# Performance work log

Measured on AMD Instinct MI355X. Metric: run time of the kernel, lower is better.

Reference implementation:

```python
import jax, jax.numpy as jnp
import numpy as np

N_NODES = 40000
N_EDGES = 640000
C = 64
NUM_GAUSS = 50
RBF_STOP = 5.0


def silu(x):
    return x * jax.nn.sigmoid(x)


def setup_inputs() -> dict:
    key = jax.random.key(0)
    ks = jax.random.split(key, 16)
    scalar = jax.random.normal(ks[0], (N_NODES, C), dtype=jnp.float32)
    vector = jax.random.normal(ks[1], (N_NODES, 3, C), dtype=jnp.float32)
    position = jax.random.normal(ks[2], (N_NODES, 3), dtype=jnp.float32)
    # avoid self-edges so dist > 0 (sqrt grad finite in bwd variant)
    row = jax.random.randint(ks[3], (N_EDGES,), 0, N_NODES, dtype=jnp.int32)
    off = jax.random.randint(ks[4], (N_EDGES,), 1, N_NODES, dtype=jnp.int32)
    col = (row + off) % N_NODES
    edge_index = jnp.stack([row, col], axis=0)
    edge_attr = jax.random.uniform(ks[5], (N_EDGES,), dtype=jnp.float32) + 0.1
    s = 1.0 / np.sqrt(2 * C)
    Ws2s = jax.random.normal(ks[6], (2 * C, C), dtype=jnp.float32) * s
    bs2s = jnp.zeros((C,), dtype=jnp.float32)
    Wv2s = jax.random.normal(ks[7], (2 * C + NUM_GAUSS, C), dtype=jnp.float32) * s
    bv2s = jnp.zeros((C,), dtype=jnp.float32)
    Wsl = jax.random.normal(ks[8], (2 * C, C), dtype=jnp.float32) * s
    bsl = jnp.zeros((C,), dtype=jnp.float32)
    Ws2v = jax.random.normal(ks[9], (2 * C, C), dtype=jnp.float32) * s
    bs2v = jnp.zeros((C,), dtype=jnp.float32)
    Wv2v = jax.random.normal(ks[10], (2 * C, C), dtype=jnp.float32) * s
    Wvl = jax.random.normal(ks[11], (2 * C, C), dtype=jnp.float32) * s
    return dict(scalar=scalar, vector=vector, position=position,
                edge_index=edge_index, edge_attr=edge_attr,
                Ws2s=Ws2s, bs2s=bs2s, Wv2s=Wv2s, bv2s=bv2s,
                Wsl=Wsl, bsl=bsl, Ws2v=Ws2v, bs2v=bs2v, Wv2v=Wv2v, Wvl=Wvl)


def _molnet_layer(scalar, vector, position, edge_index, edge_attr,
                  Ws2s, bs2s, Wv2s, bv2s, Wsl, bsl, Ws2v, bs2v, Wv2v, Wvl):
    N = scalar.shape[0]
    row, col = edge_index[0], edge_index[1]
    # B=True degree normalization: deg[c] = sum of edge_attr into c
    deg = jax.ops.segment_sum(edge_attr, col, num_segments=N)
    dis = jnp.where(deg > 0, deg ** -0.5, 0.0)
    norm = dis[row] * dis[col] * edge_attr  # [E]

    # PyG convention: _i = target (col), _j = source (row)
    si, sj = scalar[col], scalar[row]          # [E, C]
    vi, vj = vector[col], vector[row]          # [E, 3, C]
    pi, pj = position[col], position[row]      # [E, 3]

    rel = pi - pj                              # [E, 3]
    dist = jnp.sqrt(jnp.sum(rel * rel, axis=-1))  # [E]

    # GaussianSmearing(0, 5, 50)
    offset = jnp.linspace(0.0, RBF_STOP, NUM_GAUSS, dtype=scalar.dtype)
    coeff = -0.5 / (RBF_STOP / (NUM_GAUSS - 1)) ** 2
    rbf = jnp.exp(coeff * (dist[:, None] - offset[None, :]) ** 2)  # [E, 50]

    # ---- Scalar_Conv message ----
    ss = silu(jnp.concatenate([si, sj], axis=1) @ Ws2s + bs2s)  # [E, C]
    vn_i = jnp.linalg.norm(vi, axis=1)  # [E, C], norm over 3-axis
    vn_j = jnp.linalg.norm(vj, axis=1)
    vs = silu(jnp.concatenate([vn_i, vn_j, rbf], axis=-1) @ Wv2s + bv2s)  # [E, C]
    msg_s = norm[:, None] * (jnp.concatenate([ss, vs], axis=1) @ Wsl + bsl)
    agg_s = jax.ops.segment_sum(msg_s, col, num_segments=N)  # [N, C]

    # ---- Vector_Conv message ----
    vv = jnp.concatenate([vi, vj], axis=-1) @ Wv2v  # [E, 3, C], no bias
    sv = jnp.tanh(jnp.concatenate([si, sj], axis=1) @ Ws2v + bs2v)  # [E, C]
    sv = sv[:, None, :] * rel[:, :, None]  # [E, 3, C]
    msg_v = norm[:, None, None] * (jnp.concatenate([vv, sv], axis=-1) @ Wvl)
    agg_v = jax.ops.segment_sum(msg_v, col, num_segments=N)  # [N, 3, C]

    scalar_out = silu(agg_s) + scalar
    vector_out = agg_v + vector
    return scalar_out, vector_out


def reference(scalar, vector, position, edge_index, edge_attr,
              Ws2s, bs2s, Wv2s, bv2s, Wsl, bsl, Ws2v, bs2v, Wv2v, Wvl):
    return _molnet_layer(scalar, vector, position, edge_index, edge_attr,
                         Ws2s, bs2s, Wv2s, bv2s, Wsl, bsl, Ws2v, bs2v, Wv2v, Wvl)
```

## Files before the change

### kernel.cpp

```cpp
#include <hip/hip_runtime.h>


typedef __attribute__((ext_vector_type(8))) short bf16x8;
typedef __attribute__((ext_vector_type(4))) float f32x4;
#define MFMA16(a, b, c) __builtin_amdgcn_mfma_f32_16x16x32_bf16(a, b, c, 0, 0, 0)

__device__ __forceinline__ unsigned short f2bf(float x) {
    union { float f; unsigned u; } v; v.f = x;
    unsigned r = v.u + 0x7FFF + ((v.u >> 16) & 1);
    return (unsigned short)(r >> 16);
}
__device__ __forceinline__ float bf2f(unsigned short h) {
    union { unsigned u; float f; } v; v.u = ((unsigned)h) << 16; return v.f;
}
__device__ __forceinline__ float ulo(unsigned u) {
    union { unsigned u; float f; } v; v.u = u << 16; return v.f;
}
__device__ __forceinline__ float uhi(unsigned u) {
    union { unsigned u; float f; } v; v.u = u & 0xffff0000u; return v.f;
}
__device__ __forceinline__ float silu_f(float x) {
    return x * __builtin_amdgcn_rcpf(1.0f + __expf(-x));
}
__device__ __forceinline__ float tanh_f(float x) {
    return 1.0f - 2.0f * __builtin_amdgcn_rcpf(1.0f + __expf(2.0f * x));
}
__device__ __forceinline__ int rfl(int x) { return __builtin_amdgcn_readfirstlane(x); }

__global__ __launch_bounds__(256) void deg_cnt_k(const int* __restrict__ ei,
                                                 const float* __restrict__ attr,
                                                 float* __restrict__ dc, int E) {
    int e = blockIdx.x * 256 + threadIdx.x;
    if (e < E) {
        int col = ei[E + e];
        atomicAdd(&dc[2 * col], attr[e]);
        atomicAdd((int*)dc + 2 * col + 1, 1);
    }
}

__global__ __launch_bounds__(1024) void scan1_k(const float* __restrict__ dc,
                                                int* __restrict__ blockSums, int N) {
    __shared__ int tmp[1024];
    int i = blockIdx.x * 1024 + threadIdx.x;
    tmp[threadIdx.x] = (i < N) ? ((const int*)dc)[2 * i + 1] : 0;
    __syncthreads();
    for (int s = 512; s > 0; s >>= 1) {
        if (threadIdx.x < s) tmp[threadIdx.x] += tmp[threadIdx.x + s];
        __syncthreads();
    }
    if (threadIdx.x == 0) blockSums[blockIdx.x] = tmp[0];
}

__global__ __launch_bounds__(1024) void scan3_k(const float* __restrict__ dc,
                                                const int* __restrict__ blockSums,
                                                int* __restrict__ offA,
                                                int* __restrict__ offB,
                                                float* __restrict__ dis, int N) {
    __shared__ int tmp[1024];
    __shared__ int base_s;
    if (threadIdx.x == 0) {
        int b = 0;
        for (int j = 0; j < (int)blockIdx.x; ++j) b += blockSums[j];
        base_s = b;
    }
    int i = blockIdx.x * 1024 + threadIdx.x;
    tmp[threadIdx.x] = (i < N) ? ((const int*)dc)[2 * i + 1] : 0;
    __syncthreads();
    for (int s = 1; s < 1024; s <<= 1) {
        int t = (threadIdx.x >= s) ? tmp[threadIdx.x - s] : 0;
        __syncthreads();
        tmp[threadIdx.x] += t;
        __syncthreads();
    }
    if (i < N) {
        int off = base_s + tmp[threadIdx.x];
        offA[i + 1] = off;
        offB[i + 1] = off;
        float d = dc[2 * i];
        dis[i] = (d > 0.0f) ? rsqrtf(d) : 0.0f;
    }
    if (blockIdx.x == 0 && threadIdx.x == 0) { offA[0] = 0; offB[0] = 0; }
}

__global__ __launch_bounds__(256) void mid_k(
    const int* __restrict__ ei, const float* __restrict__ attr,
    const float* __restrict__ pos,
    const float* __restrict__ dis, int* __restrict__ offA,
    int2* __restrict__ PLa, float4* __restrict__ PLb, int E,
    const float* __restrict__ scalar, const float* __restrict__ vec,
    unsigned short* __restrict__ X, unsigned short* __restrict__ R2, int N,
    const float* __restrict__ Ws2s, const float* __restrict__ Ws2v,
    const float* __restrict__ Wv2s, const float* __restrict__ Wsl,
    const float* __restrict__ Wvl, const float* __restrict__ Wv2v,
    unsigned short* __restrict__ BT6, unsigned short* __restrict__ BTs,
    unsigned short* __restrict__ BTv, float* __restrict__ T2) {
    int idx = blockIdx.x * 256 + threadIdx.x;
    if (idx < E) {
        int row = ei[idx];
        int col = ei[E + idx];
        int p = atomicAdd(&offA[col], 1);
        float nrm = dis[col] * (dis[row] * attr[idx]);
        float r0 = pos[col * 3 + 0] - pos[row * 3 + 0];
        float r1 = pos[col * 3 + 1] - pos[row * 3 + 1];
        float r2 = pos[col * 3 + 2] - pos[row * 3 + 2];
        float d2 = r0 * r0 + r1 * r1 + r2 * r2;
        float t = fminf(sqrtf(d2) * (512.0f / 6.0f), 511.0f);
        PLa[p] = make_int2(row * 192, __float_as_int(nrm));
        PLb[p] = make_float4(r0, r1, r2, t);
        return;
    }
    idx -= E;
    if (idx < N * 64) {
        int n = idx >> 6, c = idx & 63;
        float v0 = vec[(size_t)n * 192 + c];
        float v1 = vec[(size_t)n * 192 + 64 + c];
        float v2 = vec[(size_t)n * 192 + 128 + c];
        X[(size_t)n * 128 + c] = f2bf(scalar[(size_t)n * 64 + c]);
        X[(size_t)n * 128 + 64 + c] = f2bf(sqrtf(v0 * v0 + v1 * v1 + v2 * v2));
        unsigned short* rw = R2 + (size_t)n * 384 + c * 6;
        rw[3] = f2bf(v0);
        *(unsigned*)(rw + 4) = (unsigned)f2bf(v1) | ((unsigned)f2bf(v2) << 16);
        return;
    }
    idx -= N * 64;
    if (idx < 24576) {
        int y = idx >> 12, n = (idx >> 6) & 63, k = idx & 63;
        const float* W = (y < 2) ? Ws2s : (y < 4) ? Ws2v : Wv2s;
        int kk = (y & 1) ? (64 + k) : k;
        BT6[idx] = f2bf(W[kk * 64 + n]);
    } else if (idx < 32768) {
        int j = idx - 24576;
        int n = j >> 7, k = j & 127;
        BTs[(size_t)n * 128 + k] = f2bf(Wsl[k * 64 + n]);
    } else if (idx < 36864) {
        int j = idx - 32768;
        int n = j >> 6, k = j & 63;
        BTv[(size_t)n * 192 + k] = f2bf(Wvl[(64 + k) * 64 + n]);
    } else if (idx < 45056) {
        int j = idx - 36864;
        int half = j >> 12;
        int k = (j >> 6) & 63, c = j & 63;
        const float* Wr = Wv2v + (half ? 0 : 64 * 64) + k * 64;
        float acc = 0.0f;
        for (int m = 0; m < 64; ++m) acc += Wr[m] * Wvl[m * 64 + c];
        BTv[(size_t)c * 192 + (half ? 128 : 64) + k] = f2bf(acc);
    } else {
        int j = idx - 45056;
        if (j >= 513 * 64) return;
        int s = j >> 6, c = j & 63;
        float d = (float)s * (6.0f / 512.0f);
        float acc = 0.0f;
        for (int l = 0; l < 50; ++l) {
            float dl = d - 0.10204081632653061f * (float)l;
            acc += __expf(-48.02f * dl * dl) * Wv2s[(128 + l) * 64 + c];
        }
        T2[(s * 64 + c) * 2] = acc;
        if (s > 0) T2[((s - 1) * 64 + c) * 2 + 1] = acc;
    }
}

__global__ __launch_bounds__(256) void node_gemm_k(
    const unsigned short* __restrict__ X, const unsigned short* __restrict__ BT6,
    const float* __restrict__ bs2s, const float* __restrict__ bs2v,
    const float* __restrict__ bv2s,
    unsigned short* __restrict__ PC3, unsigned short* __restrict__ R2, int N) {
    const int lane = threadIdx.x & 63;
    const int mtile = blockIdx.x * 4 + (threadIdx.x >> 6);
    const int r0 = mtile * 16;
    if (r0 >= N) return;
    const int quad = lane >> 4, l = lane & 15;
    const int arow = min(r0 + l, N - 1);
    const unsigned short* ap = X + (size_t)arow * 128 + quad * 8;
    bf16x8 as0 = *(const bf16x8*)ap;
    bf16x8 as1 = *(const bf16x8*)(ap + 32);
    bf16x8 av0 = *(const bf16x8*)(ap + 64);
    bf16x8 av1 = *(const bf16x8*)(ap + 96);
    f32x4 acc[6][4];
#pragma unroll
    for (int y = 0; y < 6; ++y) {
        bf16x8 a0 = (y < 4) ? as0 : av0;
        bf16x8 a1 = (y < 4) ? as1 : av1;
        const unsigned short* bp = BT6 + (size_t)y * 4096 + (size_t)l * 64 + quad * 8;
#pragma unroll
        for (int nt = 0; nt < 4; ++nt) {
            acc[y][nt] = (f32x4){0.f, 0.f, 0.f, 0.f};
            bf16x8 b0 = *(const bf16x8*)(bp + nt * 1024);
            bf16x8 b1 = *(const bf16x8*)(bp + nt * 1024 + 32);
            acc[y][nt] = MFMA16(a0, b0, acc[y][nt]);
            acc[y][nt] = MFMA16(a1, b1, acc[y][nt]);
        }
    }
#pragma unroll
    for (int nt = 0; nt < 4; ++nt) {
        int col = nt * 16 + l;
        float b0 = bs2s[col], b1 = bs2v[col], b2 = bv2s[col];
#pragma unroll
        for (int i = 0; i < 4; ++i) {
            int row = r0 + quad * 4 + i;
            if (row < N) {
                unsigned short* pd = PC3 + (size_t)row * 192 + col * 3;
                pd[0] = f2bf(acc[0][nt][i] + b0);
                pd[1] = f2bf(acc[2][nt][i] + b1);
                pd[2] = f2bf(acc[4][nt][i] + b2);
                unsigned short* rd = R2 + (size_t)row * 384 + col * 6;
                *(unsigned*)rd = (unsigned)f2bf(acc[1][nt][i]) |
                                 ((unsigned)f2bf(acc[3][nt][i]) << 16);
                rd[2] = f2bf(acc[5][nt][i]);
            }
        }
    }
}

#define STG(S, EIDX)                                                       \
    {                                                                      \
        int2 pa_ = PLa[EIDX];                                              \
        float4 pb_ = PLb[EIDX];                                            \
        ro##S = rfl(pa_.x);                                                \
        nrm##S = __int_as_float(pa_.y);                                    \
        r0##S = pb_.x; r1##S = pb_.y; r2##S = pb_.z;                       \
        const unsigned* rp_ = R2u + ro##S + lane3;                         \
        u0##S = rp_[0]; u1##S = rp_[1]; u2##S = rp_[2];                    \
        int si_ = (int)pb_.w;                                              \
        fr##S = pb_.w - (float)si_;                                        \
        float2 tp_ = *(const float2*)(T2 + (si_ << 7) + lane2);            \
        tx##S = tp_.x; ty##S = tp_.y;                                      \
    }

#define CMP(S, NRMV)                                                       \
    {                                                                      \
        float ss_ = silu_f(pc0 + ulo(u0##S));                              \
        float tt_ = tanh_f(pc1 + uhi(u0##S));                              \
        float rb_ = tx##S + fr##S * (ty##S - tx##S);                       \
        float vs_ = silu_f(pc2 + ulo(u1##S) + rb_);                        \
        ws += NRMV;                                                        \
        a1 = fmaf(NRMV, ss_, a1);                                          \
        a2 = fmaf(NRMV, vs_, a2);                                          \
        float nt_ = NRMV * tt_;                                            \
        b30 = fmaf(nt_, r0##S, b30);                                       \
        b31 = fmaf(nt_, r1##S, b31);                                       \
        b32 = fmaf(nt_, r2##S, b32);                                       \
        bv0 = fmaf(NRMV, uhi(u1##S), bv0);                                 \
        bv1 = fmaf(NRMV, ulo(u2##S), bv1);                                 \
        bv2 = fmaf(NRMV, uhi(u2##S), bv2);                                 \
    }

#define TOTW 8192

__global__ __launch_bounds__(256) void edge_sorted_k(
    const unsigned short* __restrict__ PC3, const unsigned* __restrict__ R2u,
    const float* __restrict__ T2, const int2* __restrict__ PLa,
    const float4* __restrict__ PLb, const int* __restrict__ offB,
    unsigned short* __restrict__ Xs, unsigned short* __restrict__ Xv,
    float* __restrict__ Wsum, int N) {
    const int lane = threadIdx.x & 63;
    const int lane3 = lane * 3;
    const int lane2 = lane << 1;
    const int wave = rfl((blockIdx.x * 256 + threadIdx.x) >> 6);
#pragma unroll 1
    for (int col = wave; col < N; col += TOTW) {
        const int e0 = rfl(offB[col]);
        const int e1 = rfl(offB[col + 1]);
        const unsigned short* pcb = PC3 + (size_t)col * 192 + lane3;
        const float pc0 = bf2f(pcb[0]), pc1 = bf2f(pcb[1]), pc2 = bf2f(pcb[2]);
        const unsigned* rc = R2u + (size_t)col * 192 + lane3;
        const unsigned cd1 = rc[1], cd2 = rc[2];
        const float wc0 = uhi(cd1), wc1 = ulo(cd2), wc2 = uhi(cd2);
        float a1 = 0, a2 = 0, ws = 0;
        float b30 = 0, b31 = 0, b32 = 0, bv0 = 0, bv1 = 0, bv2 = 0;
        if (e0 < e1) {
            int roA, roB;
            float nrmA, r0A, r1A, r2A, frA, txA, tyA;
            float nrmB, r0B, r1B, r2B, frB, txB, tyB;
            unsigned u0A, u1A, u2A, u0B, u1B, u2B;
            STG(A, e0);
            for (int e = e0; e < e1; e += 2) {
                const int eB = (e + 1 < e1) ? (e + 1) : e;
                STG(B, eB);
                const float nB = (e + 1 < e1) ? nrmB : 0.0f;
                CMP(A, nrmA);
                if (e + 2 < e1) STG(A, e + 2);
                CMP(B, nB);
            }
        }
        Xs[(size_t)col * 128 + lane] = f2bf(a1);
        Xs[(size_t)col * 128 + 64 + lane] = f2bf(a2);
        const size_t xb = (size_t)col * 576;
        Xv[xb + lane]       = f2bf(b30);
        Xv[xb + 64 + lane]  = f2bf(bv0);
        Xv[xb + 128 + lane] = f2bf(ws * wc0);
        Xv[xb + 192 + lane] = f2bf(b31);
        Xv[xb + 256 + lane] = f2bf(bv1);
        Xv[xb + 320 + lane] = f2bf(ws * wc1);
        Xv[xb + 384 + lane] = f2bf(b32);
        Xv[xb + 448 + lane] = f2bf(bv2);
        Xv[xb + 512 + lane] = f2bf(ws * wc2);
        if (lane == 0) Wsum[col] = ws;
    }
}
#undef STG
#undef CMP

__global__ __launch_bounds__(256) void gemm_sv_k(
    const unsigned short* __restrict__ Xs, const unsigned short* __restrict__ BTs,
    const unsigned short* __restrict__ Xv, const unsigned short* __restrict__ BTv,
    const float* __restrict__ bsl, const float* __restrict__ Wsum,
    const float* __restrict__ scalar, const float* __restrict__ vec,
    float* __restrict__ outs, float* __restrict__ outv, int N) {
    const int y = blockIdx.y;
    const int lane = threadIdx.x & 63;
    const int quad = lane >> 4, l = lane & 15;
    const int wave = threadIdx.x >> 6;
    if (y == 0) {
        const int r0 = (blockIdx.x * 4 + wave) * 16;
        if (r0 >= N) return;
        const int arow = min(r0 + l, N - 1);
        const unsigned short* aptr = Xs + (size_t)arow * 128 + quad * 8;
        bf16x8 a[4];
#pragma unroll
        for (int s = 0; s < 4; ++s) a[s] = *(const bf16x8*)(aptr + s * 32);
        const unsigned short* bptr = BTs + (size_t)l * 128 + quad * 8;
        f32x4 acc[4];
#pragma unroll
        for (int nt = 0; nt < 4; ++nt) {
            acc[nt] = (f32x4){0.f, 0.f, 0.f, 0.f};
#pragma unroll
            for (int s = 0; s < 4; ++s) {
                bf16x8 b = *(const bf16x8*)(bptr + (size_t)nt * 16 * 128 + s * 32);
                acc[nt] = MFMA16(a[s], b, acc[nt]);
            }
        }
#pragma unroll
        for (int nt = 0; nt < 4; ++nt) {
            int col = nt * 16 + l;
            float bc = bsl[col];
#pragma unroll
            for (int i = 0; i < 4; ++i) {
                int row = r0 + quad * 4 + i;
                if (row < N) {
                    float wsn = Wsum[row];
                    outs[(size_t)row * 64 + col] =
                        silu_f(acc[nt][i] + wsn * bc) + scalar[(size_t)row * 64 + col];
                }
            }
        }
    } else {
        const int M = 3 * N;
        const int r0 = ((y - 1) * (N / 16) + blockIdx.x * 4 + wave) * 16;
        if (r0 >= M) return;
        const int arow = min(r0 + l, M - 1);
        const unsigned short* aptr = Xv + (size_t)arow * 192 + quad * 8;
        bf16x8 a[6];
#pragma unroll
        for (int s = 0; s < 6; ++s) a[s] = *(const bf16x8*)(aptr + s * 32);
        const unsigned short* bptr = BTv + (size_t)l * 192 + quad * 8;
        f32x4 acc[4];
#pragma unroll
        for (int nt = 0; nt < 4; ++nt) {
            acc[nt] = (f32x4){0.f, 0.f, 0.f, 0.f};
#pragma unroll
            for (int s = 0; s < 6; ++s) {
                bf16x8 b = *(const bf16x8*)(bptr + (size_t)nt * 16 * 192 + s * 32);
                acc[nt] = MFMA16(a[s], b, acc[nt]);
            }
        }
#pragma unroll
        for (int nt = 0; nt < 4; ++nt) {
            int col = nt * 16 + l;
#pragma unroll
            for (int i = 0; i < 4; ++i) {
                int row = r0 + quad * 4 + i;
                if (row < M)
                    outv[(size_t)row * 64 + col] = acc[nt][i] + vec[(size_t)row * 64 + col];
            }
        }
    }
}

extern "C" void kernel_launch(void* const* d_in, const int* in_sizes, int n_in,
                              void* d_out, int out_size, void* d_ws, size_t ws_size,
                              hipStream_t stream) {
    const float* scalar     = (const float*)d_in[0];
    const float* vector     = (const float*)d_in[1];
    const float* position   = (const float*)d_in[2];
    const int*   edge_index = (const int*)d_in[3];
    const float* edge_attr  = (const float*)d_in[4];
    const float* Ws2s       = (const float*)d_in[5];
    const float* bs2s       = (const float*)d_in[6];
    const float* Wv2s       = (const float*)d_in[7];
    const float* bv2s       = (const float*)d_in[8];
    const float* Wsl        = (const float*)d_in[9];
    const float* bsl        = (const float*)d_in[10];
    const float* Ws2v       = (const float*)d_in[11];
    const float* bs2v       = (const float*)d_in[12];
    const float* Wv2v       = (const float*)d_in[13];
    const float* Wvl        = (const float*)d_in[14];

    const int N = in_sizes[0] / 64;
    const int E = in_sizes[3] / 2;
    const size_t sN = (size_t)N;
    const int nb = (N + 1023) / 1024;

    float* W = (float*)d_ws;
    float*          dis  = W;
    unsigned short* X    = (unsigned short*)(W + sN);
    unsigned short* Xs   = X;
    unsigned short* R2   = (unsigned short*)(W + 65 * sN);
    unsigned short* PC3  = (unsigned short*)(W + 257 * sN);
    unsigned short* Xv   = (unsigned short*)(W + 353 * sN);
    float* dc        = W + 353 * sN;
    int*   offA      = (int*)(W + 355 * sN);
    int*   blockSums = (int*)(W + 357 * sN);
    unsigned short* BT6 = (unsigned short*)(W + 358 * sN);
    float* Wsum = W + 641 * sN;
    int*   offB = (int*)(W + 642 * sN);
    unsigned short* BTs = (unsigned short*)(W + 644 * sN);
    unsigned short* BTv = (unsigned short*)(W + 644 * sN + 4096);
    float* T2   = W + 644 * sN + 10240;
    int2*  PLa  = (int2*)(W + 646 * sN);

    float* outs = (float*)d_out;
    float* outv = outs + 64 * sN;
    float4* PLb = (float4*)(outs + 64 * sN);

    hipMemsetAsync(dc, 0, sizeof(float) * 2 * sN, stream);

    deg_cnt_k<<<(E + 255) / 256, 256, 0, stream>>>(edge_index, edge_attr, dc, E);
    scan1_k<<<nb, 1024, 0, stream>>>(dc, blockSums, N);
    scan3_k<<<nb, 1024, 0, stream>>>(dc, blockSums, offA, offB, dis, N);

    const int midTot = E + N * 64 + 45056 + 513 * 64;
    mid_k<<<(midTot + 255) / 256, 256, 0, stream>>>(
        edge_index, edge_attr, position, dis, offA, PLa, PLb, E,
        scalar, vector, X, R2, N,
        Ws2s, Ws2v, Wv2s, Wsl, Wvl, Wv2v, BT6, BTs, BTv, T2);

    const int mtilesN = (N + 15) / 16;
    node_gemm_k<<<(mtilesN + 3) / 4, 256, 0, stream>>>(
        X, BT6, bs2s, bs2v, bv2s, PC3, R2, N);

    edge_sorted_k<<<TOTW / 4, 256, 0, stream>>>(
        PC3, (const unsigned*)R2, T2, PLa, PLb, offB, Xs, Xv, Wsum, N);

    gemm_sv_k<<<dim3((mtilesN + 3) / 4, 4), 256, 0, stream>>>(
        Xs, BTs, Xv, BTv, bsl, Wsum, scalar, vector, outs, outv, N);
}
```

Before: 385.5 us.

## Pack per-edge payload into one 32B record and de-interleave R2 rows

Merges the two per-edge arrays (int2 PLa plus float4 PLb) into a single 32-byte record of two float4s, stored at the start of the output buffer. It also changes the R2 node row layout from per-lane interleaved triples (lane*3) to three planar 64-word segments, so each gather of a source node's row becomes three coalesced per-lane word loads. The aim is to reduce scattered memory transactions in the edge-gather kernel, at the cost of writing 32 rather than 24 bytes per edge and more strided stores in the producer kernels.

```diff
diff --git a/kernel.cpp b/kernel.cpp
--- a/kernel.cpp
+++ b/kernel.cpp
@@ -86,7 +86,7 @@
     const int* __restrict__ ei, const float* __restrict__ attr,
     const float* __restrict__ pos,
     const float* __restrict__ dis, int* __restrict__ offA,
-    int2* __restrict__ PLa, float4* __restrict__ PLb, int E,
+    float4* __restrict__ PLq, int E,
     const float* __restrict__ scalar, const float* __restrict__ vec,
     unsigned short* __restrict__ X, unsigned short* __restrict__ R2, int N,
     const float* __restrict__ Ws2s, const float* __restrict__ Ws2v,
@@ -105,8 +105,8 @@
         float r2 = pos[col * 3 + 2] - pos[row * 3 + 2];
         float d2 = r0 * r0 + r1 * r1 + r2 * r2;
         float t = fminf(sqrtf(d2) * (512.0f / 6.0f), 511.0f);
-        PLa[p] = make_int2(row * 192, __float_as_int(nrm));
-        PLb[p] = make_float4(r0, r1, r2, t);
+        PLq[2 * p]     = make_float4(__int_as_float(row * 192), nrm, r0, r1);
+        PLq[2 * p + 1] = make_float4(r2, t, 0.0f, 0.0f);
         return;
     }
     idx -= E;
@@ -117,9 +117,10 @@
         float v2 = vec[(size_t)n * 192 + 128 + c];
         X[(size_t)n * 128 + c] = f2bf(scalar[(size_t)n * 64 + c]);
         X[(size_t)n * 128 + 64 + c] = f2bf(sqrtf(v0 * v0 + v1 * v1 + v2 * v2));
-        unsigned short* rw = R2 + (size_t)n * 384 + c * 6;
-        rw[3] = f2bf(v0);
-        *(unsigned*)(rw + 4) = (unsigned)f2bf(v1) | ((unsigned)f2bf(v2) << 16);
+        unsigned short* rb = R2 + (size_t)n * 384;
+        rb[128 + 2 * c + 1] = f2bf(v0);
+        *(unsigned*)(rb + 256 + 2 * c) =
+            (unsigned)f2bf(v1) | ((unsigned)f2bf(v2) << 16);
         return;
     }
     idx -= N * 64;
@@ -202,10 +203,11 @@
                 pd[0] = f2bf(acc[0][nt][i] + b0);
                 pd[1] = f2bf(acc[2][nt][i] + b1);
                 pd[2] = f2bf(acc[4][nt][i] + b2);
-                unsigned short* rd = R2 + (size_t)row * 384 + col * 6;
-                *(unsigned*)rd = (unsigned)f2bf(acc[1][nt][i]) |
-                                 ((unsigned)f2bf(acc[3][nt][i]) << 16);
-                rd[2] = f2bf(acc[5][nt][i]);
+                unsigned short* rd = R2 + (size_t)row * 384;
+                *(unsigned*)(rd + 2 * col) =
+                    (unsigned)f2bf(acc[1][nt][i]) |
+                    ((unsigned)f2bf(acc[3][nt][i]) << 16);
+                rd[128 + 2 * col] = f2bf(acc[5][nt][i]);
             }
         }
     }
@@ -213,15 +215,15 @@
 
 #define STG(S, EIDX)                                                       \
     {                                                                      \
-        int2 pa_ = PLa[EIDX];                                              \
-        float4 pb_ = PLb[EIDX];                                            \
-        ro##S = rfl(pa_.x);                                                \
-        nrm##S = __int_as_float(pa_.y);                                    \
-        r0##S = pb_.x; r1##S = pb_.y; r2##S = pb_.z;                       \
-        const unsigned* rp_ = R2u + ro##S + lane3;                         \
-        u0##S = rp_[0]; u1##S = rp_[1]; u2##S = rp_[2];                    \
-        int si_ = (int)pb_.w;                                              \
-        fr##S = pb_.w - (float)si_;                                        \
+        const float4 pa_ = PLq[2 * (EIDX)];                                \
+        const float4 pb_ = PLq[2 * (EIDX) + 1];                            \
+        ro##S = rfl(__float_as_int(pa_.x));                                \
+        nrm##S = pa_.y;                                                    \
+        r0##S = pa_.z; r1##S = pa_.w; r2##S = pb_.x;                       \
+        const unsigned* rp_ = R2u + ro##S;                                 \
+        u0##S = rp_[lane]; u1##S = rp_[64 + lane]; u2##S = rp_[128 + lane];\
+        int si_ = (int)pb_.y;                                              \
+        fr##S = pb_.y - (float)si_;                                        \
         float2 tp_ = *(const float2*)(T2 + (si_ << 7) + lane2);            \
         tx##S = tp_.x; ty##S = tp_.y;                                      \
     }
@@ -248,8 +250,8 @@
 
 __global__ __launch_bounds__(256) void edge_sorted_k(
     const unsigned short* __restrict__ PC3, const unsigned* __restrict__ R2u,
-    const float* __restrict__ T2, const int2* __restrict__ PLa,
-    const float4* __restrict__ PLb, const int* __restrict__ offB,
+    const float* __restrict__ T2, const float4* __restrict__ PLq,
+    const int* __restrict__ offB,
     unsigned short* __restrict__ Xs, unsigned short* __restrict__ Xv,
     float* __restrict__ Wsum, int N) {
     const int lane = threadIdx.x & 63;
@@ -262,8 +264,8 @@
         const int e1 = rfl(offB[col + 1]);
         const unsigned short* pcb = PC3 + (size_t)col * 192 + lane3;
         const float pc0 = bf2f(pcb[0]), pc1 = bf2f(pcb[1]), pc2 = bf2f(pcb[2]);
-        const unsigned* rc = R2u + (size_t)col * 192 + lane3;
-        const unsigned cd1 = rc[1], cd2 = rc[2];
+        const unsigned cd1 = R2u[(size_t)col * 192 + 64 + lane];
+        const unsigned cd2 = R2u[(size_t)col * 192 + 128 + lane];
         const float wc0 = uhi(cd1), wc1 = ulo(cd2), wc2 = uhi(cd2);
         float a1 = 0, a2 = 0, ws = 0;
         float b30 = 0, b31 = 0, b32 = 0, bv0 = 0, bv1 = 0, bv2 = 0;
@@ -416,11 +418,10 @@
     unsigned short* BTs = (unsigned short*)(W + 644 * sN);
     unsigned short* BTv = (unsigned short*)(W + 644 * sN + 4096);
     float* T2   = W + 644 * sN + 10240;
-    int2*  PLa  = (int2*)(W + 646 * sN);
 
     float* outs = (float*)d_out;
     float* outv = outs + 64 * sN;
-    float4* PLb = (float4*)(outs + 64 * sN);
+    float4* PLq = (float4*)d_out;
 
     hipMemsetAsync(dc, 0, sizeof(float) * 2 * sN, stream);
 
@@ -430,7 +431,7 @@
 
     const int midTot = E + N * 64 + 45056 + 513 * 64;
     mid_k<<<(midTot + 255) / 256, 256, 0, stream>>>(
-        edge_index, edge_attr, position, dis, offA, PLa, PLb, E,
+        edge_index, edge_attr, position, dis, offA, PLq, E,
         scalar, vector, X, R2, N,
         Ws2s, Ws2v, Wv2s, Wsl, Wvl, Wv2v, BT6, BTs, BTv, T2);
 
@@ -439,7 +440,7 @@
         X, BT6, bs2s, bs2v, bv2s, PC3, R2, N);
 
     edge_sorted_k<<<TOTW / 4, 256, 0, stream>>>(
-        PC3, (const unsigned*)R2, T2, PLa, PLb, offB, Xs, Xv, Wsum, N);
+        PC3, (const unsigned*)R2, T2, PLq, offB, Xs, Xv, Wsum, N);
 
     gemm_sv_k<<<dim3((mtilesN + 3) / 4, 4), 256, 0, stream>>>(
         Xs, BTs, Xv, BTv, bsl, Wsum, scalar, vector, outs, outv, N);
```

Measured after the change: 375.8 us. -2.5%, faster.
